# Kernel tuning notes

Measured on AMD Instinct MI355X. Metric: run time of the kernel, lower is better.

Reference implementation:

```python
import jax, jax.numpy as jnp
import numpy as np

N_NODES = 100000
N_EDGES = 1200000
D_IN, D_H, D_OUT = 64, 128, 64


def sage_conv(x, src, dst, Wl, bl, Wr):
    # PyG SAGEConv (mean aggr): out = lin_l(mean_{j in N(i)} x_j) + lin_r(x_i)
    n = x.shape[0]
    agg = jax.ops.segment_sum(x[src], dst, num_segments=n)          # [N, d]
    cnt = jax.ops.segment_sum(jnp.ones((src.shape[0],), x.dtype), dst, num_segments=n)
    mean = agg / jnp.maximum(cnt, 1.0)[:, None]
    return mean @ Wl + bl + x @ Wr


def setup_inputs() -> dict:
    key = jax.random.key(0)
    ks = jax.random.split(key, 10)

    def init_w(k, shape):
        lim = 1.0 / np.sqrt(shape[0])
        return jax.random.uniform(k, shape, jnp.float32, -lim, lim)

    return {
        "x": jax.random.normal(ks[0], (N_NODES, D_IN), jnp.float32),
        "edge_index": jax.random.randint(ks[1], (2, N_EDGES), 0, N_NODES),
        "Wl1": init_w(ks[2], (D_IN, D_H)), "bl1": jnp.zeros((D_H,), jnp.float32),
        "Wr1": init_w(ks[3], (D_IN, D_H)),
        "Wl2": init_w(ks[4], (D_H, D_OUT)), "bl2": jnp.zeros((D_OUT,), jnp.float32),
        "Wr2": init_w(ks[5], (D_H, D_OUT)),
        "W1": init_w(ks[6], (D_OUT, D_H)), "b1": jnp.zeros((D_H,), jnp.float32),
        "W2": init_w(ks[7], (D_H, 1)), "b2": jnp.zeros((1,), jnp.float32),
    }


def reference(x, edge_index, Wl1, bl1, Wr1, Wl2, bl2, Wr2, W1, b1, W2, b2):
    src, dst = edge_index[0], edge_index[1]
    h = sage_conv(x, src, dst, Wl1, bl1, Wr1)   # [N, D_H] (no activation in original)
    h = sage_conv(h, src, dst, Wl2, bl2, Wr2)   # [N, D_OUT]
    e = h[src] * h[dst]                          # [E, D_OUT] edge embeddings
    e = jax.nn.relu(e @ W1 + b1)                 # [E, D_H]
    return e @ W2 + b2                           # [E, 1] link logits
```

## Files before the change

kernel.cpp:

```cpp
#include <hip/hip_runtime.h>


typedef _Float16 f16x8 __attribute__((ext_vector_type(8)));
typedef float f32x4 __attribute__((ext_vector_type(4)));

union H4 { _Float16 h[4]; uint2 u; };
union H8 { _Float16 h[8]; uint4 u; };

__device__ inline uint2 pack4(float4 v) {
  H4 p;
  p.h[0] = (_Float16)v.x; p.h[1] = (_Float16)v.y;
  p.h[2] = (_Float16)v.z; p.h[3] = (_Float16)v.w;
  return p.u;
}

__global__ void kA_convert_hist(const float* __restrict__ x, _Float16* __restrict__ x16,
                                const int* __restrict__ dst, int* __restrict__ deg,
                                int n4, int E) {
  int t = blockIdx.x * blockDim.x + threadIdx.x;
  if (t < n4) {
    float4 v = ((const float4*)x)[t];
    ((uint2*)x16)[t] = pack4(v);
  }
  if (t < E) atomicAdd(&deg[dst[t]], 1);
}

__global__ void k_scan1(const int* __restrict__ deg, int* __restrict__ ex,
                        int* __restrict__ bsum, int N) {
  __shared__ int sm[256];
  int t = threadIdx.x, i = blockIdx.x * 256 + t;
  int v = (i < N) ? deg[i] : 0;
  sm[t] = v;
  __syncthreads();
  for (int s = 1; s < 256; s <<= 1) {
    int a = (t >= s) ? sm[t - s] : 0;
    __syncthreads();
    sm[t] += a;
    __syncthreads();
  }
  if (i < N) ex[i] = sm[t] - v;
  if (t == 255) bsum[blockIdx.x] = sm[255];
}

__global__ void k_scan2(int* __restrict__ bsum, int nb) {
  __shared__ int sm[1024];
  int t = threadIdx.x;
  int v = (t < nb) ? bsum[t] : 0;
  sm[t] = v;
  __syncthreads();
  for (int s = 1; s < 1024; s <<= 1) {
    int a = (t >= s) ? sm[t - s] : 0;
    __syncthreads();
    sm[t] += a;
    __syncthreads();
  }
  if (t < nb) bsum[t] = sm[t] - v;
}

__global__ void k_scan3(const int* __restrict__ bsum, int* __restrict__ row,
                        const int* __restrict__ ex, int N, int E) {
  int i = blockIdx.x * blockDim.x + threadIdx.x;
  if (i < N) row[i] = ex[i] + bsum[i >> 8];
  if (i == 0) row[N] = E;
}

__global__ void k_cbinit(const int* __restrict__ row, int* __restrict__ cbcursor,
                         int N, int ncb) {
  int b = threadIdx.x + blockIdx.x * blockDim.x;
  if (b < ncb) {
    int node = b << 8;
    cbcursor[b] = row[node < N ? node : N];
  }
}

__global__ __launch_bounds__(256) void k_coarse(
    const int* __restrict__ src, const int* __restrict__ dst,
    int* __restrict__ cbcursor, unsigned long long* __restrict__ ep, int E) {
  __shared__ int lh[512];
  const int t = threadIdx.x;
  const int chunk = (E + gridDim.x - 1) / gridDim.x;
  const int e0 = blockIdx.x * chunk;
  const int e1 = min(e0 + chunk, E);
  lh[t] = 0; lh[t + 256] = 0;
  __syncthreads();
  for (int e = e0 + t; e < e1; e += 256)
    atomicAdd(&lh[dst[e] >> 8], 1);
  __syncthreads();
  {
    int c0 = lh[t], c1 = lh[t + 256];
    int b0 = c0 ? atomicAdd(&cbcursor[t], c0) : 0;
    int b1 = c1 ? atomicAdd(&cbcursor[t + 256], c1) : 0;
    __syncthreads();
    lh[t] = b0; lh[t + 256] = b1;
  }
  __syncthreads();
  for (int e = e0 + t; e < e1; e += 256) {
    int d = dst[e];
    int pos = atomicAdd(&lh[d >> 8], 1);
    ep[pos] = ((unsigned long long)d << 32) | (unsigned)src[e];
  }
}

#define FS_CAP 4608
__global__ __launch_bounds__(256) void k_fine_sort(
    const unsigned long long* __restrict__ ep, const int* __restrict__ row,
    int* __restrict__ srcs, int N, int E) {
  __shared__ int cnt[256];
  __shared__ int cur[256];
  __shared__ int sm[256];
  __shared__ int stage[FS_CAP];
  const int b = blockIdx.x;
  const int t = threadIdx.x;
  const int n0 = b << 8;
  const int n1 = min(n0 + 256, N);
  const int beg = row[n0];
  const int end = row[n1];
  const int M = end - beg;

  cnt[t] = 0;
  __syncthreads();
  for (int i = beg + t; i < end; i += 256) {
    int loc = (int)(ep[i] >> 32) & 255;
    atomicAdd(&cnt[loc], 1);
  }
  __syncthreads();
  int v = cnt[t];
  sm[t] = v;
  __syncthreads();
  for (int s = 1; s < 256; s <<= 1) {
    int a = (t >= s) ? sm[t - s] : 0;
    __syncthreads();
    sm[t] += a;
    __syncthreads();
  }
  cur[t] = sm[t] - v;
  __syncthreads();
  for (int i = beg + t; i < end; i += 256) {
    unsigned long long p = ep[i];
    int loc = (int)(p >> 32) & 255;
    int pos = atomicAdd(&cur[loc], 1);
    if (pos < FS_CAP) stage[pos] = (int)(unsigned)p;
    else srcs[beg + pos] = (int)(unsigned)p;
  }
  __syncthreads();
  const int m = min(M, FS_CAP);
  for (int i = t; i < m; i += 256) srcs[beg + i] = stage[i];
}

__global__ __launch_bounds__(256) void k_gather16(
    const _Float16* __restrict__ feat, const int* __restrict__ row,
    const int* __restrict__ srcs, _Float16* __restrict__ agg, int N) {
  int tid = blockIdx.x * blockDim.x + threadIdx.x;
  int node = tid >> 3, slot = tid & 7;
  if (node >= N) return;
  int beg = row[node], end = row[node + 1];
  float acc[8];
#pragma unroll
  for (int i = 0; i < 8; i++) acc[i] = 0.f;
  int k = beg;
  for (; k + 3 < end; k += 4) {
    int s0 = srcs[k], s1 = srcs[k + 1], s2 = srcs[k + 2], s3 = srcs[k + 3];
    H8 a, b, c, d;
    a.u = *(const uint4*)(feat + (size_t)s0 * 64 + slot * 8);
    b.u = *(const uint4*)(feat + (size_t)s1 * 64 + slot * 8);
    c.u = *(const uint4*)(feat + (size_t)s2 * 64 + slot * 8);
    d.u = *(const uint4*)(feat + (size_t)s3 * 64 + slot * 8);
#pragma unroll
    for (int i = 0; i < 8; i++)
      acc[i] += ((float)a.h[i] + (float)b.h[i]) + ((float)c.h[i] + (float)d.h[i]);
  }
  for (; k < end; k++) {
    H8 a; a.u = *(const uint4*)(feat + (size_t)srcs[k] * 64 + slot * 8);
#pragma unroll
    for (int i = 0; i < 8; i++) acc[i] += (float)a.h[i];
  }
  H8 o;
#pragma unroll
  for (int i = 0; i < 8; i++) o.h[i] = (_Float16)acc[i];
  *(uint4*)(agg + (size_t)node * 64 + slot * 8) = o.u;
}

template <int K, int J, int MODE>
__global__ __launch_bounds__(256) void k_node_mfma(
    const _Float16* __restrict__ A, const _Float16* __restrict__ A2,
    const float* __restrict__ W, const float* __restrict__ Wb,
    const float* __restrict__ bias, const _Float16* __restrict__ add64,
    const int* __restrict__ deg, _Float16* __restrict__ outp, int N) {
  constexpr int KS = K / 32;
  constexpr int TT = J / 16;
  constexpr int RU4 = J / 8;
  __shared__ _Float16 ostage[4][16][J + 8];

  const int w = threadIdx.x >> 6;
  const int l = threadIdx.x & 63;
  const int col = l & 15;
  const int kb8 = (l >> 4) * 8;
  const int nb = blockIdx.x * 64 + w * 16;

  f16x8 wf[TT][KS];
#pragma unroll
  for (int tt = 0; tt < TT; tt++)
#pragma unroll
    for (int s = 0; s < KS; s++) {
      f16x8 v;
#pragma unroll
      for (int e = 0; e < 8; e++)
        v[e] = (_Float16)W[(size_t)(s * 32 + kb8 + e) * J + tt * 16 + col];
      wf[tt][s] = v;
    }

  const int nodeA = min(nb + col, N - 1);
  f16x8 af[KS];
#pragma unroll
  for (int s = 0; s < KS; s++)
    af[s] = *(const f16x8*)(A + (size_t)nodeA * K + s * 32 + kb8);

  f32x4 acc[TT];
#pragma unroll
  for (int tt = 0; tt < TT; tt++) {
    f32x4 a = {0.f, 0.f, 0.f, 0.f};
#pragma unroll
    for (int s = 0; s < KS; s++)
      a = __builtin_amdgcn_mfma_f32_16x16x32_f16(af[s], wf[tt][s], a, 0, 0, 0);
    acc[tt] = a;
  }

  if constexpr (MODE == 0) {
    float inv[4];
#pragma unroll
    for (int reg = 0; reg < 4; reg++) {
      int nd = min(nb + (l >> 4) * 4 + reg, N - 1);
      inv[reg] = 1.0f / fmaxf((float)deg[nd], 1.0f);
    }
#pragma unroll
    for (int tt = 0; tt < TT; tt++)
#pragma unroll
      for (int reg = 0; reg < 4; reg++) acc[tt][reg] *= inv[reg];

    f16x8 wfb[TT][KS];
#pragma unroll
    for (int tt = 0; tt < TT; tt++)
#pragma unroll
      for (int s = 0; s < KS; s++) {
        f16x8 v;
#pragma unroll
        for (int e = 0; e < 8; e++)
          v[e] = (_Float16)Wb[(size_t)(s * 32 + kb8 + e) * J + tt * 16 + col];
        wfb[tt][s] = v;
      }
#pragma unroll
    for (int s = 0; s < KS; s++)
      af[s] = *(const f16x8*)(A2 + (size_t)nodeA * K + s * 32 + kb8);
#pragma unroll
    for (int tt = 0; tt < TT; tt++)
#pragma unroll
      for (int s = 0; s < KS; s++)
        acc[tt] = __builtin_amdgcn_mfma_f32_16x16x32_f16(af[s], wfb[tt][s], acc[tt], 0, 0, 0);

#pragma unroll
    for (int tt = 0; tt < TT; tt++) {
      float bl = bias[tt * 16 + col];
#pragma unroll
      for (int reg = 0; reg < 4; reg++) acc[tt][reg] += bl;
    }
  }

  if constexpr (MODE == 2) {
    float inv[4];
    int ndc[4];
#pragma unroll
    for (int reg = 0; reg < 4; reg++) {
      ndc[reg] = min(nb + (l >> 4) * 4 + reg, N - 1);
      inv[reg] = 1.0f / fmaxf((float)deg[ndc[reg]], 1.0f);
    }
#pragma unroll
    for (int tt = 0; tt < TT; tt++) {
      float bl = bias[tt * 16 + col];
#pragma unroll
      for (int reg = 0; reg < 4; reg++) {
        float ad = (float)add64[(size_t)ndc[reg] * J + tt * 16 + col];
        acc[tt][reg] += ad * inv[reg] + bl;
      }
    }
  }

#pragma unroll
  for (int tt = 0; tt < TT; tt++)
#pragma unroll
    for (int reg = 0; reg < 4; reg++)
      ostage[w][(l >> 4) * 4 + reg][tt * 16 + col] = (_Float16)acc[tt][reg];
  __syncthreads();
#pragma unroll
  for (int i = 0; i < J / 32; i++) {
    int idx = i * 64 + l;
    int r = idx / RU4, q = idx % RU4;
    int gn = nb + r;
    if (gn < N)
      *(uint4*)(outp + (size_t)gn * J + q * 8) = *(const uint4*)(&ostage[w][r][q * 8]);
  }
}

__global__ __launch_bounds__(256) void k_edge_mfma(
    const _Float16* __restrict__ h2, const int* __restrict__ src,
    const int* __restrict__ dst,
    const float* __restrict__ W1, const float* __restrict__ W2,
    const float* __restrict__ b1, const float* __restrict__ b2,
    float* __restrict__ out, int E) {
  const int gtid = blockIdx.x * blockDim.x + threadIdx.x;
  const int wave = gtid >> 6;
  const int nwaves = (gridDim.x * blockDim.x) >> 6;
  const int l = threadIdx.x & 63;
  const int col = l & 15;
  const int kb = (l >> 4) * 8;
  const int hb = (l >> 4) * 4;
  const int ngroups = (E + 15) / 16;
  const int gpw = (ngroups + nwaves - 1) / nwaves;
  const int g0 = wave * gpw;
  const int g1 = min(g0 + gpw, ngroups);
  if (g0 >= ngroups) return;

  f16x8 afrag[8][2];
#pragma unroll
  for (int tt = 0; tt < 8; tt++)
#pragma unroll
    for (int s = 0; s < 2; s++) {
      f16x8 bf;
#pragma unroll
      for (int e = 0; e < 8; e++)
        bf[e] = (_Float16)W1[(size_t)(s * 32 + kb + e) * 128 + tt * 16 + col];
      afrag[tt][s] = bf;
    }
  float4 c0[8], w2v[8];
#pragma unroll
  for (int tt = 0; tt < 8; tt++) {
    int hbase = tt * 16 + hb;
    c0[tt]  = make_float4(b1[hbase], b1[hbase + 1], b1[hbase + 2], b1[hbase + 3]);
    w2v[tt] = make_float4(W2[hbase], W2[hbase + 1], W2[hbase + 2], W2[hbase + 3]);
  }
  const float b2v = b2[0];

  auto ldrows = [&](int g, f16x8& a0, f16x8& a1) {
    int pos = g * 16 + col;
    if (pos >= E) pos = E - 1;
    int sp = src[pos], dp = dst[pos];
    f16x8 as0 = *(const f16x8*)(h2 + (size_t)sp * 64 + kb);
    f16x8 ad0 = *(const f16x8*)(h2 + (size_t)dp * 64 + kb);
    f16x8 as1 = *(const f16x8*)(h2 + (size_t)sp * 64 + 32 + kb);
    f16x8 ad1 = *(const f16x8*)(h2 + (size_t)dp * 64 + 32 + kb);
    a0 = as0 * ad0;
    a1 = as1 * ad1;
  };

  auto compute = [&](int g, f16x8 a0, f16x8 a1) {
    float psum = 0.f;
#pragma unroll
    for (int tt = 0; tt < 8; tt++) {
      f32x4 acc = {c0[tt].x, c0[tt].y, c0[tt].z, c0[tt].w};
      acc = __builtin_amdgcn_mfma_f32_16x16x32_f16(afrag[tt][0], a0, acc, 0, 0, 0);
      acc = __builtin_amdgcn_mfma_f32_16x16x32_f16(afrag[tt][1], a1, acc, 0, 0, 0);
      psum += fmaxf(acc[0], 0.f) * w2v[tt].x + fmaxf(acc[1], 0.f) * w2v[tt].y
            + fmaxf(acc[2], 0.f) * w2v[tt].z + fmaxf(acc[3], 0.f) * w2v[tt].w;
    }
    psum += __shfl_xor(psum, 16, 64);
    psum += __shfl_xor(psum, 32, 64);
    if (l < 16) {
      int epos = g * 16 + l;
      if (epos < E) out[epos] = psum + b2v;
    }
  };

  f16x8 a0, a1, na0, na1;
  ldrows(g0, a0, a1);
  for (int g = g0; g < g1; g++) {
    if (g + 1 < g1) ldrows(g + 1, na0, na1);
    compute(g, a0, a1);
    a0 = na0; a1 = na1;
  }
}

extern "C" void kernel_launch(void* const* d_in, const int* in_sizes, int n_in,
                              void* d_out, int out_size, void* d_ws, size_t ws_size,
                              hipStream_t stream) {
  const float* x   = (const float*)d_in[0];
  const int*   ei  = (const int*)d_in[1];
  const float* Wl1 = (const float*)d_in[2];
  const float* bl1 = (const float*)d_in[3];
  const float* Wr1 = (const float*)d_in[4];
  const float* Wl2 = (const float*)d_in[5];
  const float* bl2 = (const float*)d_in[6];
  const float* Wr2 = (const float*)d_in[7];
  const float* W1  = (const float*)d_in[8];
  const float* b1  = (const float*)d_in[9];
  const float* W2  = (const float*)d_in[10];
  const float* b2  = (const float*)d_in[11];
  const int N = in_sizes[0] / 64;
  const int E = in_sizes[1] / 2;
  const int* src = ei;
  const int* dstp = ei + E;

  char* w = (char*)d_ws;
  size_t off = 0;
  auto alloc = [&](size_t bytes) -> void* {
    void* p = w + off;
    off = (off + bytes + 255) & ~(size_t)255;
    return p;
  };
  int*      deg      = (int*)alloc((size_t)N * 4);
  int*      row      = (int*)alloc((size_t)(N + 1) * 4);
  int*      ex       = (int*)alloc((size_t)N * 4);
  int*      bsum     = (int*)alloc(1024 * 4);
  int*      cbcursor = (int*)alloc(512 * 4);
  int*      srcs     = (int*)alloc((size_t)E * 4);
  unsigned long long* ep = (unsigned long long*)alloc((size_t)E * 8);
  _Float16* f16buf   = (_Float16*)alloc((size_t)N * 64 * 2);
  _Float16* agg16    = (_Float16*)alloc((size_t)N * 64 * 2);
  _Float16* h1_16    = (_Float16*)alloc((size_t)N * 128 * 2);

  const int ncb = (N + 255) >> 8;

  hipMemsetAsync(deg, 0, (size_t)N * 4, stream);
  int n4 = N * 16;
  int kag = (max(n4, E) + 255) / 256;
  kA_convert_hist<<<kag, 256, 0, stream>>>(x, f16buf, dstp, deg, n4, E);
  int nb = (N + 255) / 256;
  k_scan1<<<nb, 256, 0, stream>>>(deg, ex, bsum, N);
  k_scan2<<<1, 1024, 0, stream>>>(bsum, nb);
  k_scan3<<<nb, 256, 0, stream>>>(bsum, row, ex, N, E);
  k_cbinit<<<2, 256, 0, stream>>>(row, cbcursor, N, ncb);
  k_coarse<<<256, 256, 0, stream>>>(src, dstp, cbcursor, ep, E);
  k_fine_sort<<<ncb, 256, 0, stream>>>(ep, row, srcs, N, E);

  int ngrid = (N + 63) / 64;
  int ggrid = (N * 8 + 255) / 256;
  k_gather16<<<ggrid, 256, 0, stream>>>(f16buf, row, srcs, agg16, N);
  k_node_mfma<64, 128, 0><<<ngrid, 256, 0, stream>>>(
      agg16, f16buf, Wl1, Wr1, bl1, nullptr, deg, h1_16, N);
  k_node_mfma<128, 64, 1><<<ngrid, 256, 0, stream>>>(
      h1_16, nullptr, Wl2, nullptr, nullptr, nullptr, nullptr, f16buf, N);
  k_gather16<<<ggrid, 256, 0, stream>>>(f16buf, row, srcs, agg16, N);
  k_node_mfma<128, 64, 2><<<ngrid, 256, 0, stream>>>(
      h1_16, nullptr, Wr2, nullptr, bl2, agg16, deg, f16buf, N);
  k_edge_mfma<<<4096, 256, 0, stream>>>(f16buf, src, dstp, W1, W2, b1, b2,
                                        (float*)d_out, E);
}
```

Baseline: 273.4 us.

## Store gathered node features in feature-sliced layout for cache-friendly gathers

Measured after the change: 338.6 us. 1.24x slower.

```diff
diff --git a/kernel.cpp b/kernel.cpp
--- a/kernel.cpp
+++ b/kernel.cpp
@@ -7,20 +7,22 @@
 union H4 { _Float16 h[4]; uint2 u; };
 union H8 { _Float16 h[8]; uint4 u; };
 
-__device__ inline uint2 pack4(float4 v) {
-  H4 p;
-  p.h[0] = (_Float16)v.x; p.h[1] = (_Float16)v.y;
-  p.h[2] = (_Float16)v.z; p.h[3] = (_Float16)v.w;
-  return p.u;
-}
-
-__global__ void kA_convert_hist(const float* __restrict__ x, _Float16* __restrict__ x16,
-                                const int* __restrict__ dst, int* __restrict__ deg,
-                                int n4, int E) {
+__global__ __launch_bounds__(256) void kA_slice_hist(
+    const float* __restrict__ x, _Float16* __restrict__ xs,
+    const int* __restrict__ dst, int* __restrict__ deg, int N, int E) {
   int t = blockIdx.x * blockDim.x + threadIdx.x;
-  if (t < n4) {
-    float4 v = ((const float4*)x)[t];
-    ((uint2*)x16)[t] = pack4(v);
+  if (t < N) {
+    const float4* xv = (const float4*)(x + (size_t)t * 64);
+#pragma unroll
+    for (int sl = 0; sl < 8; sl++) {
+      float4 a = xv[2 * sl], b = xv[2 * sl + 1];
+      H8 p;
+      p.h[0] = (_Float16)a.x; p.h[1] = (_Float16)a.y;
+      p.h[2] = (_Float16)a.z; p.h[3] = (_Float16)a.w;
+      p.h[4] = (_Float16)b.x; p.h[5] = (_Float16)b.y;
+      p.h[6] = (_Float16)b.z; p.h[7] = (_Float16)b.w;
+      *(uint4*)(xs + ((size_t)sl * N + t) * 8) = p.u;
+    }
   }
   if (t < E) atomicAdd(&deg[dst[t]], 1);
 }
@@ -147,12 +149,13 @@
   for (int i = t; i < m; i += 256) srcs[beg + i] = stage[i];
 }
 
-__global__ __launch_bounds__(256) void k_gather16(
-    const _Float16* __restrict__ feat, const int* __restrict__ row,
-    const int* __restrict__ srcs, _Float16* __restrict__ agg, int N) {
-  int tid = blockIdx.x * blockDim.x + threadIdx.x;
-  int node = tid >> 3, slot = tid & 7;
+__global__ __launch_bounds__(256) void k_gather_slice(
+    const _Float16* __restrict__ xs, const int* __restrict__ row,
+    const int* __restrict__ srcs, _Float16* __restrict__ ags, int N) {
+  const int sl = blockIdx.x & 7;
+  const int node = (blockIdx.x >> 3) * 256 + threadIdx.x;
   if (node >= N) return;
+  const _Float16* xsl = xs + (size_t)sl * N * 8;
   int beg = row[node], end = row[node + 1];
   float acc[8];
 #pragma unroll
@@ -161,26 +164,26 @@
   for (; k + 3 < end; k += 4) {
     int s0 = srcs[k], s1 = srcs[k + 1], s2 = srcs[k + 2], s3 = srcs[k + 3];
     H8 a, b, c, d;
-    a.u = *(const uint4*)(feat + (size_t)s0 * 64 + slot * 8);
-    b.u = *(const uint4*)(feat + (size_t)s1 * 64 + slot * 8);
-    c.u = *(const uint4*)(feat + (size_t)s2 * 64 + slot * 8);
-    d.u = *(const uint4*)(feat + (size_t)s3 * 64 + slot * 8);
+    a.u = *(const uint4*)(xsl + (size_t)s0 * 8);
+    b.u = *(const uint4*)(xsl + (size_t)s1 * 8);
+    c.u = *(const uint4*)(xsl + (size_t)s2 * 8);
+    d.u = *(const uint4*)(xsl + (size_t)s3 * 8);
 #pragma unroll
     for (int i = 0; i < 8; i++)
       acc[i] += ((float)a.h[i] + (float)b.h[i]) + ((float)c.h[i] + (float)d.h[i]);
   }
   for (; k < end; k++) {
-    H8 a; a.u = *(const uint4*)(feat + (size_t)srcs[k] * 64 + slot * 8);
+    H8 a; a.u = *(const uint4*)(xsl + (size_t)srcs[k] * 8);
 #pragma unroll
     for (int i = 0; i < 8; i++) acc[i] += (float)a.h[i];
   }
   H8 o;
 #pragma unroll
   for (int i = 0; i < 8; i++) o.h[i] = (_Float16)acc[i];
-  *(uint4*)(agg + (size_t)node * 64 + slot * 8) = o.u;
-}
-
-template <int K, int J, int MODE>
+  *(uint4*)(ags + ((size_t)sl * N + node) * 8) = o.u;
+}
+
+template <int K, int J, int MODE, int ASLICE, int OSLICE>
 __global__ __launch_bounds__(256) void k_node_mfma(
     const _Float16* __restrict__ A, const _Float16* __restrict__ A2,
     const float* __restrict__ W, const float* __restrict__ Wb,
@@ -196,6 +199,14 @@
   const int col = l & 15;
   const int kb8 = (l >> 4) * 8;
   const int nb = blockIdx.x * 64 + w * 16;
+  const int nodeA = min(nb + col, N - 1);
+
+  auto loadA = [&](const _Float16* __restrict__ S, int s) -> f16x8 {
+    if constexpr (ASLICE)
+      return *(const f16x8*)(S + ((size_t)(s * 4 + (kb8 >> 3)) * N + nodeA) * 8);
+    else
+      return *(const f16x8*)(S + (size_t)nodeA * K + s * 32 + kb8);
+  };
 
   f16x8 wf[TT][KS];
 #pragma unroll
@@ -209,11 +220,9 @@
       wf[tt][s] = v;
     }
 
-  const int nodeA = min(nb + col, N - 1);
   f16x8 af[KS];
 #pragma unroll
-  for (int s = 0; s < KS; s++)
-    af[s] = *(const f16x8*)(A + (size_t)nodeA * K + s * 32 + kb8);
+  for (int s = 0; s < KS; s++) af[s] = loadA(A, s);
 
   f32x4 acc[TT];
 #pragma unroll
@@ -249,8 +258,7 @@
         wfb[tt][s] = v;
       }
 #pragma unroll
-    for (int s = 0; s < KS; s++)
-      af[s] = *(const f16x8*)(A2 + (size_t)nodeA * K + s * 32 + kb8);
+    for (int s = 0; s < KS; s++) af[s] = loadA(A2, s);
 #pragma unroll
     for (int tt = 0; tt < TT; tt++)
 #pragma unroll
@@ -276,9 +284,11 @@
 #pragma unroll
     for (int tt = 0; tt < TT; tt++) {
       float bl = bias[tt * 16 + col];
+      int jsl = tt * 2 + (col >> 3);
+      int jd  = col & 7;
 #pragma unroll
       for (int reg = 0; reg < 4; reg++) {
-        float ad = (float)add64[(size_t)ndc[reg] * J + tt * 16 + col];
+        float ad = (float)add64[((size_t)jsl * N + ndc[reg]) * 8 + jd];
         acc[tt][reg] += ad * inv[reg] + bl;
       }
     }
@@ -290,13 +300,26 @@
     for (int reg = 0; reg < 4; reg++)
       ostage[w][(l >> 4) * 4 + reg][tt * 16 + col] = (_Float16)acc[tt][reg];
   __syncthreads();
-#pragma unroll
-  for (int i = 0; i < J / 32; i++) {
-    int idx = i * 64 + l;
-    int r = idx / RU4, q = idx % RU4;
-    int gn = nb + r;
-    if (gn < N)
-      *(uint4*)(outp + (size_t)gn * J + q * 8) = *(const uint4*)(&ostage[w][r][q * 8]);
+  if constexpr (OSLICE) {
+#pragma unroll
+    for (int i = 0; i < 2; i++) {
+      int idx = i * 64 + l;
+      int q = idx >> 4, r = idx & 15;
+      int gn = nb + r;
+      if (gn < N)
+        *(uint4*)(outp + ((size_t)q * N + gn) * 8) =
+            *(const uint4*)(&ostage[w][r][q * 8]);
+    }
+  } else {
+#pragma unroll
+    for (int i = 0; i < J / 32; i++) {
+      int idx = i * 64 + l;
+      int r = idx / RU4, q = idx % RU4;
+      int gn = nb + r;
+      if (gn < N)
+        *(uint4*)(outp + (size_t)gn * J + q * 8) =
+            *(const uint4*)(&ostage[w][r][q * 8]);
+    }
   }
 }
 
@@ -413,15 +436,15 @@
   int*      srcs     = (int*)alloc((size_t)E * 4);
   unsigned long long* ep = (unsigned long long*)alloc((size_t)E * 8);
   _Float16* f16buf   = (_Float16*)alloc((size_t)N * 64 * 2);
-  _Float16* agg16    = (_Float16*)alloc((size_t)N * 64 * 2);
+  _Float16* xs       = (_Float16*)alloc((size_t)N * 64 * 2);
+  _Float16* ags      = (_Float16*)alloc((size_t)N * 64 * 2);
   _Float16* h1_16    = (_Float16*)alloc((size_t)N * 128 * 2);
 
   const int ncb = (N + 255) >> 8;
 
   hipMemsetAsync(deg, 0, (size_t)N * 4, stream);
-  int n4 = N * 16;
-  int kag = (max(n4, E) + 255) / 256;
-  kA_convert_hist<<<kag, 256, 0, stream>>>(x, f16buf, dstp, deg, n4, E);
+  int kag = (max(N, E) + 255) / 256;
+  kA_slice_hist<<<kag, 256, 0, stream>>>(x, xs, dstp, deg, N, E);
   int nb = (N + 255) / 256;
   k_scan1<<<nb, 256, 0, stream>>>(deg, ex, bsum, N);
   k_scan2<<<1, 1024, 0, stream>>>(bsum, nb);
@@ -431,15 +454,15 @@
   k_fine_sort<<<ncb, 256, 0, stream>>>(ep, row, srcs, N, E);
 
   int ngrid = (N + 63) / 64;
-  int ggrid = (N * 8 + 255) / 256;
-  k_gather16<<<ggrid, 256, 0, stream>>>(f16buf, row, srcs, agg16, N);
-  k_node_mfma<64, 128, 0><<<ngrid, 256, 0, stream>>>(
-      agg16, f16buf, Wl1, Wr1, bl1, nullptr, deg, h1_16, N);
-  k_node_mfma<128, 64, 1><<<ngrid, 256, 0, stream>>>(
-      h1_16, nullptr, Wl2, nullptr, nullptr, nullptr, nullptr, f16buf, N);
-  k_gather16<<<ggrid, 256, 0, stream>>>(f16buf, row, srcs, agg16, N);
-  k_node_mfma<128, 64, 2><<<ngrid, 256, 0, stream>>>(
-      h1_16, nullptr, Wr2, nullptr, bl2, agg16, deg, f16buf, N);
+  int sgrid = 8 * ((N + 255) / 256);
+  k_gather_slice<<<sgrid, 256, 0, stream>>>(xs, row, srcs, ags, N);
+  k_node_mfma<64, 128, 0, 1, 0><<<ngrid, 256, 0, stream>>>(
+      ags, xs, Wl1, Wr1, bl1, nullptr, deg, h1_16, N);
+  k_node_mfma<128, 64, 1, 0, 1><<<ngrid, 256, 0, stream>>>(
+      h1_16, nullptr, Wl2, nullptr, nullptr, nullptr, nullptr, xs, N);
+  k_gather_slice<<<sgrid, 256, 0, stream>>>(xs, row, srcs, ags, N);
+  k_node_mfma<128, 64, 2, 0, 0><<<ngrid, 256, 0, stream>>>(
+      h1_16, nullptr, Wr2, nullptr, bl2, ags, deg, f16buf, N);
   k_edge_mfma<<<4096, 256, 0, stream>>>(f16buf, src, dstp, W1, W2, b1, b2,
                                         (float*)d_out, E);
 }
```
